# Kernel optimization log

Measured on AMD Instinct MI355X. Metric: run time of the kernel, lower is better.

Reference implementation:

```python
import jax, jax.numpy as jnp
import numpy as np


def setup_inputs() -> dict:
    key = jax.random.key(0)
    ks = jax.random.split(key, 7)
    B, S, D, R = 4, 4096, 1024, 16
    scale = 1.0 / np.sqrt(D)
    return {
        "x": jax.random.normal(ks[0], (B, S, D), dtype=jnp.float32),
        "W_qkv": jax.random.normal(ks[1], (3 * D, D), dtype=jnp.float32) * scale,
        "b_qkv": jax.random.normal(ks[2], (3 * D,), dtype=jnp.float32) * 0.02,
        "W_a_q": jax.random.normal(ks[3], (R, D), dtype=jnp.float32) * scale,
        "W_b_q": jnp.zeros((D, R), dtype=jnp.float32) + jax.random.normal(ks[4], (D, R), dtype=jnp.float32) * 0.02,
        "W_a_v": jax.random.normal(ks[5], (R, D), dtype=jnp.float32) * scale,
        "W_b_v": jax.random.normal(ks[6], (D, R), dtype=jnp.float32) * 0.02,
    }


def reference(x, W_qkv, b_qkv, W_a_q, W_b_q, W_a_v, W_b_v):
    D = W_a_q.shape[1]
    # base qkv projection: [B, S, 3D]
    qkv = jnp.einsum("bsd,ed->bse", x, W_qkv) + b_qkv
    # LoRA branches: x -> [B,S,r] -> [B,S,D]
    q_ba = jnp.einsum("bsr,dr->bsd", jnp.einsum("bsd,rd->bsr", x, W_a_q), W_b_q)
    v_ba = jnp.einsum("bsr,dr->bsd", jnp.einsum("bsd,rd->bsr", x, W_a_v), W_b_v)
    # add into q slice ([:D]) and v slice ([-D:])
    qkv = qkv.at[:, :, :D].add(q_ba)
    qkv = qkv.at[:, :, -D:].add(v_ba)
    return qkv
```

## Files before the change

### kernel.cpp

```cpp
#include <hip/hip_runtime.h>
#include <hip/hip_bf16.h>

typedef __bf16 bf16x4 __attribute__((ext_vector_type(4)));
typedef __bf16 bf16x8 __attribute__((ext_vector_type(8)));
typedef float floatx4 __attribute__((ext_vector_type(4)));

#define GLD16(gp, lp) __builtin_amdgcn_global_load_lds(                      \
    (const __attribute__((address_space(1))) void*)(gp),                     \
    (__attribute__((address_space(3))) void*)(lp), 16, 0, 0)

constexpr int Mdim = 16384;
constexpr int Ndim = 3072;
constexpr int Kdim = 1024;

static __device__ __forceinline__ bf16x8 cvt8(floatx4 lo, floatx4 hi) {
    bf16x8 r;
#pragma unroll
    for (int e = 0; e < 4; ++e) { r[e] = (__bf16)lo[e]; r[e + 4] = (__bf16)hi[e]; }
    return r;
}


__global__ __launch_bounds__(256) void build_weff(
    const float* __restrict__ Wqkv,
    const float* __restrict__ Waq,
    const float* __restrict__ Wbq,
    const float* __restrict__ Wav,
    const float* __restrict__ Wbv,
    __hip_bfloat16* __restrict__ Weff)
{
    const int idx = (blockIdx.x * 256 + threadIdx.x) * 4;
    const int e = idx >> 10;
    const int d = idx & 1023;
    floatx4 v = *(const floatx4*)(Wqkv + idx);
    if (e < 1024) {
#pragma unroll
        for (int r = 0; r < 16; ++r) {
            const float wb = Wbq[e * 16 + r];
            floatx4 wa = *(const floatx4*)(Waq + r * 1024 + d);
#pragma unroll
            for (int q = 0; q < 4; ++q) v[q] += wb * wa[q];
        }
    } else if (e >= 2048) {
        const int e2 = e - 2048;
#pragma unroll
        for (int r = 0; r < 16; ++r) {
            const float wb = Wbv[e2 * 16 + r];
            floatx4 wa = *(const floatx4*)(Wav + r * 1024 + d);
#pragma unroll
            for (int q = 0; q < 4; ++q) v[q] += wb * wa[q];
        }
    }
    bf16x4 o;
#pragma unroll
    for (int q = 0; q < 4; ++q) o[q] = (__bf16)v[q];
    *(bf16x4*)(Weff + idx) = o;
}

__global__ __launch_bounds__(256) void cvt_x(
    const float* __restrict__ x, __hip_bfloat16* __restrict__ xb)
{
    const size_t idx = ((size_t)blockIdx.x * 256 + threadIdx.x) * 8;
    bf16x8 r = cvt8(*(const floatx4*)(x + idx), *(const floatx4*)(x + idx + 4));
    *(bf16x8*)(xb + idx) = r;
}

__global__ __launch_bounds__(256, 3) void gemm_bf16(
    const __hip_bfloat16* __restrict__ A,
    const __hip_bfloat16* __restrict__ Bw,
    const float* __restrict__ bias,
    float* __restrict__ C)
{
    constexpr int TK = 32;
    __shared__ __hip_bfloat16 As[128 * TK];
    __shared__ __hip_bfloat16 Bs[128 * TK];

    const int t    = threadIdx.x;
    const int wave = t >> 6;
    const int lane = t & 63;
    const int bx   = blockIdx.x % (Ndim / 128);
    const int by   = blockIdx.x / (Ndim / 128);
    const int m0   = by * 128;
    const int n0   = bx * 128;
    const int wm   = wave >> 1;
    const int wn   = wave & 1;

    const int srow = wave * 16 + (lane >> 2);
    const int scol = (lane & 3) * 8;

    const __hip_bfloat16* Ag0 = A  + (size_t)(m0 + srow) * Kdim + scol;
    const __hip_bfloat16* Ag1 = Ag0 + (size_t)64 * Kdim;
    const __hip_bfloat16* Bg0 = Bw + (size_t)(n0 + srow) * Kdim + scol;
    const __hip_bfloat16* Bg1 = Bg0 + (size_t)64 * Kdim;

    __hip_bfloat16* Al0 = &As[srow * TK + scol];
    __hip_bfloat16* Al1 = &As[(srow + 64) * TK + scol];
    __hip_bfloat16* Bl0 = &Bs[srow * TK + scol];
    __hip_bfloat16* Bl1 = &Bs[(srow + 64) * TK + scol];

    const int fm = lane & 15;
    const int fk = (lane >> 4) * 8;

    floatx4 acc[4][4];
#pragma unroll
    for (int i = 0; i < 4; ++i)
#pragma unroll
        for (int j = 0; j < 4; ++j)
            acc[i][j] = (floatx4){0.f, 0.f, 0.f, 0.f};

    for (int kt = 0; kt < Kdim; kt += TK) {
        GLD16(Ag0 + kt, Al0);
        GLD16(Ag1 + kt, Al1);
        GLD16(Bg0 + kt, Bl0);
        GLD16(Bg1 + kt, Bl1);
        __syncthreads();

        bf16x8 af[4], bfr[4];
#pragma unroll
        for (int i = 0; i < 4; ++i) {
            af[i]  = *(const bf16x8*)&As[(wm * 64 + i * 16 + fm) * TK + fk];
            bfr[i] = *(const bf16x8*)&Bs[(wn * 64 + i * 16 + fm) * TK + fk];
        }
#pragma unroll
        for (int i = 0; i < 4; ++i)
#pragma unroll
            for (int j = 0; j < 4; ++j)
                acc[i][j] = __builtin_amdgcn_mfma_f32_16x16x32_bf16(af[i], bfr[j], acc[i][j], 0, 0, 0);
        __syncthreads();
    }

    const int cn = lane & 15;
    const int cm = (lane >> 4) * 4;
    float bv[4];
#pragma unroll
    for (int j = 0; j < 4; ++j)
        bv[j] = bias[n0 + wn * 64 + j * 16 + cn];

#pragma unroll
    for (int i = 0; i < 4; ++i) {
        const int m = m0 + wm * 64 + i * 16 + cm;
#pragma unroll
        for (int j = 0; j < 4; ++j) {
            const int n = n0 + wn * 64 + j * 16 + cn;
            const size_t base = (size_t)m * Ndim + n;
#pragma unroll
            for (int r = 0; r < 4; ++r)
                C[base + (size_t)r * Ndim] = acc[i][j][r] + bv[j];
        }
    }
}


__global__ __launch_bounds__(256, 2) void gemm_bias_f32(
    const float* __restrict__ A, const float* __restrict__ Bw,
    const float* __restrict__ bias, float* __restrict__ C)
{
    constexpr int TK = 32;
    __shared__ __hip_bfloat16 As[128 * TK];
    __shared__ __hip_bfloat16 Bs[128 * TK];

    const int t    = threadIdx.x;
    const int wave = t >> 6;
    const int lane = t & 63;
    const int bx   = blockIdx.x % (Ndim / 128);
    const int by   = blockIdx.x / (Ndim / 128);
    const int m0   = by * 128;
    const int n0   = bx * 128;
    const int wm   = wave >> 1;
    const int wn   = wave & 1;
    const int srow = wave * 16 + (lane >> 2);
    const int scol = (lane & 3) * 8;

    const float* Ag0 = A  + (size_t)(m0 + srow) * Kdim + scol;
    const float* Ag1 = Ag0 + (size_t)64 * Kdim;
    const float* Bg0 = Bw + (size_t)(n0 + srow) * Kdim + scol;
    const float* Bg1 = Bg0 + (size_t)64 * Kdim;

    __hip_bfloat16* Al0 = &As[srow * TK + scol];
    __hip_bfloat16* Al1 = &As[(srow + 64) * TK + scol];
    __hip_bfloat16* Bl0 = &Bs[srow * TK + scol];
    __hip_bfloat16* Bl1 = &Bs[(srow + 64) * TK + scol];

    const int fm = lane & 15;
    const int fk = (lane >> 4) * 8;

    floatx4 acc[4][4];
#pragma unroll
    for (int i = 0; i < 4; ++i)
#pragma unroll
        for (int j = 0; j < 4; ++j)
            acc[i][j] = (floatx4){0.f, 0.f, 0.f, 0.f};

    for (int kt = 0; kt < Kdim; kt += TK) {
        bf16x8 a0 = cvt8(*(const floatx4*)(Ag0 + kt), *(const floatx4*)(Ag0 + kt + 4));
        bf16x8 a1 = cvt8(*(const floatx4*)(Ag1 + kt), *(const floatx4*)(Ag1 + kt + 4));
        bf16x8 b0 = cvt8(*(const floatx4*)(Bg0 + kt), *(const floatx4*)(Bg0 + kt + 4));
        bf16x8 b1 = cvt8(*(const floatx4*)(Bg1 + kt), *(const floatx4*)(Bg1 + kt + 4));
        __syncthreads();
        *(bf16x8*)Al0 = a0;
        *(bf16x8*)Al1 = a1;
        *(bf16x8*)Bl0 = b0;
        *(bf16x8*)Bl1 = b1;
        __syncthreads();

        bf16x8 af[4], bfr[4];
#pragma unroll
        for (int i = 0; i < 4; ++i) {
            af[i]  = *(const bf16x8*)&As[(wm * 64 + i * 16 + fm) * TK + fk];
            bfr[i] = *(const bf16x8*)&Bs[(wn * 64 + i * 16 + fm) * TK + fk];
        }
#pragma unroll
        for (int i = 0; i < 4; ++i)
#pragma unroll
            for (int j = 0; j < 4; ++j)
                acc[i][j] = __builtin_amdgcn_mfma_f32_16x16x32_bf16(af[i], bfr[j], acc[i][j], 0, 0, 0);
    }

    const int cn = lane & 15;
    const int cm = (lane >> 4) * 4;
    float bv[4];
#pragma unroll
    for (int j = 0; j < 4; ++j)
        bv[j] = bias[n0 + wn * 64 + j * 16 + cn];
#pragma unroll
    for (int i = 0; i < 4; ++i) {
        const int m = m0 + wm * 64 + i * 16 + cm;
#pragma unroll
        for (int j = 0; j < 4; ++j) {
            const int n = n0 + wn * 64 + j * 16 + cn;
            const size_t base = (size_t)m * Ndim + n;
#pragma unroll
            for (int r = 0; r < 4; ++r)
                C[base + (size_t)r * Ndim] = acc[i][j][r] + bv[j];
        }
    }
}

__global__ __launch_bounds__(256) void lora_rmw(
    const float* __restrict__ x,
    const float* __restrict__ Waq, const float* __restrict__ Wbq,
    const float* __restrict__ Wav, const float* __restrict__ Wbv,
    float* __restrict__ out)
{
    __shared__ float Pq[64][16];
    __shared__ float Pv[64][16];
    const int t  = threadIdx.x;
    const int m0 = blockIdx.x * 64;
    {
        const int row = t >> 2;
        const int r0  = (t & 3) * 4;
        float accq[4] = {0.f, 0.f, 0.f, 0.f};
        float accv[4] = {0.f, 0.f, 0.f, 0.f};
        const float* xr = x + (size_t)(m0 + row) * Kdim;
        for (int d = 0; d < Kdim; d += 4) {
            floatx4 xv = *(const floatx4*)(xr + d);
#pragma unroll
            for (int rr = 0; rr < 4; ++rr) {
                floatx4 wq = *(const floatx4*)(Waq + (size_t)(r0 + rr) * Kdim + d);
                floatx4 wv = *(const floatx4*)(Wav + (size_t)(r0 + rr) * Kdim + d);
#pragma unroll
                for (int e = 0; e < 4; ++e) {
                    accq[rr] += xv[e] * wq[e];
                    accv[rr] += xv[e] * wv[e];
                }
            }
        }
#pragma unroll
        for (int rr = 0; rr < 4; ++rr) {
            Pq[row][r0 + rr] = accq[rr];
            Pv[row][r0 + rr] = accv[rr];
        }
    }
    __syncthreads();
    const int col  = t * 8;
    const bool isq = col < 1024;
    const int nn0  = isq ? col : col - 1024;
    const int n    = isq ? col : col + 1024;
    const float* Wb = isq ? Wbq : Wbv;
    for (int row = 0; row < 64; ++row) {
        const float* P = isq ? Pq[row] : Pv[row];
        const size_t off = (size_t)(m0 + row) * Ndim + n;
        floatx4 o0 = *(const floatx4*)(out + off);
        floatx4 o1 = *(const floatx4*)(out + off + 4);
#pragma unroll
        for (int i = 0; i < 8; ++i) {
            floatx4 w0 = *(const floatx4*)(Wb + (size_t)(nn0 + i) * 16);
            floatx4 w1 = *(const floatx4*)(Wb + (size_t)(nn0 + i) * 16 + 4);
            floatx4 w2 = *(const floatx4*)(Wb + (size_t)(nn0 + i) * 16 + 8);
            floatx4 w3 = *(const floatx4*)(Wb + (size_t)(nn0 + i) * 16 + 12);
            float s = 0.f;
#pragma unroll
            for (int r = 0; r < 4; ++r)
                s += P[r] * w0[r] + P[r + 4] * w1[r] + P[r + 8] * w2[r] + P[r + 12] * w3[r];
            if (i < 4) o0[i] += s; else o1[i - 4] += s;
        }
        *(floatx4*)(out + off)     = o0;
        *(floatx4*)(out + off + 4) = o1;
    }
}

extern "C" void kernel_launch(void* const* d_in, const int* in_sizes, int n_in,
                              void* d_out, int out_size, void* d_ws, size_t ws_size,
                              hipStream_t stream)
{
    (void)in_sizes; (void)n_in; (void)out_size;
    const float* x    = (const float*)d_in[0];
    const float* Wqkv = (const float*)d_in[1];
    const float* bqkv = (const float*)d_in[2];
    const float* Waq  = (const float*)d_in[3];
    const float* Wbq  = (const float*)d_in[4];
    const float* Wav  = (const float*)d_in[5];
    const float* Wbv  = (const float*)d_in[6];
    float* out = (float*)d_out;

    const size_t WEFF_BYTES = (size_t)Ndim * Kdim * sizeof(__hip_bfloat16);
    const size_t XB_BYTES   = (size_t)Mdim * Kdim * sizeof(__hip_bfloat16);

    if (ws_size >= WEFF_BYTES + XB_BYTES) {
        __hip_bfloat16* Weff = (__hip_bfloat16*)d_ws;
        __hip_bfloat16* xb   = (__hip_bfloat16*)((char*)d_ws + WEFF_BYTES);
        build_weff<<<(Ndim * Kdim / 4) / 256, 256, 0, stream>>>(Wqkv, Waq, Wbq, Wav, Wbv, Weff);
        cvt_x<<<(int)(((size_t)Mdim * Kdim / 8) / 256), 256, 0, stream>>>(x, xb);
        gemm_bf16<<<(Mdim / 128) * (Ndim / 128), 256, 0, stream>>>(xb, Weff, bqkv, out);
    } else {
        gemm_bias_f32<<<(Mdim / 128) * (Ndim / 128), 256, 0, stream>>>(x, Wqkv, bqkv, out);
        lora_rmw<<<Mdim / 64, 256, 0, stream>>>(x, Waq, Wbq, Wav, Wbv, out);
    }
}
```

Measured before the change: 382.2 us.

## Rewrite bf16 GEMM as 256x256 double-buffered 8-phase pipelined kernel

Replaces the 128x128, 256-thread, K-step-32 GEMM with a 256x256 tile kernel using 512 threads and K-step 64. Each K tile is double-buffered in LDS with an XOR swizzle. Global-to-LDS staging of the next tile is interleaved between four MFMA sub-phases, with s_setprio raising the priority of the MFMA sections. Block IDs are also remapped to improve L2 locality. The goal is to hide load latency, raise data reuse per LDS byte, and cut bank conflicts, at the cost of 128KB of LDS per block, which limits occupancy to one block per CU.

Measured after the change: 366.9 us. -4.0%, faster.

```diff
diff --git a/kernel.cpp b/kernel.cpp
--- a/kernel.cpp
+++ b/kernel.cpp
@@ -65,68 +65,116 @@
     *(bf16x8*)(xb + idx) = r;
 }
 
-__global__ __launch_bounds__(256, 3) void gemm_bf16(
+__global__ __launch_bounds__(512, 2) void gemm_bf16_8ph(
     const __hip_bfloat16* __restrict__ A,
     const __hip_bfloat16* __restrict__ Bw,
     const float* __restrict__ bias,
     float* __restrict__ C)
 {
-    constexpr int TK = 32;
-    __shared__ __hip_bfloat16 As[128 * TK];
-    __shared__ __hip_bfloat16 Bs[128 * TK];
+    constexpr int NT = Kdim / 64;
+    __shared__ __hip_bfloat16 lds[2][2][256 * 64];
 
     const int t    = threadIdx.x;
-    const int wave = t >> 6;
+    const int wid  = t >> 6;
     const int lane = t & 63;
-    const int bx   = blockIdx.x % (Ndim / 128);
-    const int by   = blockIdx.x / (Ndim / 128);
-    const int m0   = by * 128;
-    const int n0   = bx * 128;
-    const int wm   = wave >> 1;
-    const int wn   = wave & 1;
-
-    const int srow = wave * 16 + (lane >> 2);
-    const int scol = (lane & 3) * 8;
-
-    const __hip_bfloat16* Ag0 = A  + (size_t)(m0 + srow) * Kdim + scol;
-    const __hip_bfloat16* Ag1 = Ag0 + (size_t)64 * Kdim;
-    const __hip_bfloat16* Bg0 = Bw + (size_t)(n0 + srow) * Kdim + scol;
-    const __hip_bfloat16* Bg1 = Bg0 + (size_t)64 * Kdim;
-
-    __hip_bfloat16* Al0 = &As[srow * TK + scol];
-    __hip_bfloat16* Al1 = &As[(srow + 64) * TK + scol];
-    __hip_bfloat16* Bl0 = &Bs[srow * TK + scol];
-    __hip_bfloat16* Bl1 = &Bs[(srow + 64) * TK + scol];
-
-    const int fm = lane & 15;
-    const int fk = (lane >> 4) * 8;
-
-    floatx4 acc[4][4];
-#pragma unroll
-    for (int i = 0; i < 4; ++i)
+    const int wm   = wid >> 2;
+    const int wn   = wid & 3;
+
+    constexpr int NWG = (Mdim / 256) * (Ndim / 256);
+    const int bid = (blockIdx.x & 7) * (NWG >> 3) + (blockIdx.x >> 3);
+    const int bx  = bid % (Ndim / 256);
+    const int by  = bid / (Ndim / 256);
+    const int m0  = by * 256;
+    const int n0  = bx * 256;
+
+    const int srow0 = t >> 3;
+    const int scb_s = ((t & 7) * 16) ^ ((srow0 & 7) << 4);
+
+#define STAGE_HALF(G, R0, h, nb_, mat, kt_) do {                               \
+    const __hip_bfloat16* _g = (G) + (size_t)((R0) + (h) * 128 + srow0) * Kdim \
+                               + (kt_) * 64 + (scb_s >> 1);                    \
+    char* _l = (char*)&lds[nb_][mat][0] + (h) * 16384 + t * 16;                \
+    GLD16(_g, _l);                                                             \
+    GLD16(_g + (size_t)64 * Kdim, _l + 8192);                                  \
+} while (0)
+
+    const int fm   = lane & 15;
+    const int fk2  = (lane >> 4) * 16;
+    const int fxor = (fm & 7) << 4;
+    const int cbs0 = fk2 ^ fxor;
+    const int cbs1 = (64 + fk2) ^ fxor;
+
+    floatx4 acc[8][4];
+#pragma unroll
+    for (int i = 0; i < 8; ++i)
 #pragma unroll
         for (int j = 0; j < 4; ++j)
             acc[i][j] = (floatx4){0.f, 0.f, 0.f, 0.f};
 
-    for (int kt = 0; kt < Kdim; kt += TK) {
-        GLD16(Ag0 + kt, Al0);
-        GLD16(Ag1 + kt, Al1);
-        GLD16(Bg0 + kt, Bl0);
-        GLD16(Bg1 + kt, Bl1);
-        __syncthreads();
-
-        bf16x8 af[4], bfr[4];
-#pragma unroll
-        for (int i = 0; i < 4; ++i) {
-            af[i]  = *(const bf16x8*)&As[(wm * 64 + i * 16 + fm) * TK + fk];
-            bfr[i] = *(const bf16x8*)&Bs[(wn * 64 + i * 16 + fm) * TK + fk];
-        }
-#pragma unroll
-        for (int i = 0; i < 4; ++i)
-#pragma unroll
-            for (int j = 0; j < 4; ++j)
-                acc[i][j] = __builtin_amdgcn_mfma_f32_16x16x32_bf16(af[i], bfr[j], acc[i][j], 0, 0, 0);
-        __syncthreads();
+#define MFMA_QUAD(mq, nq, BQ)                                                  \
+    __builtin_amdgcn_s_setprio(1);                                             \
+    _Pragma("unroll")                                                          \
+    for (int i = 0; i < 4; ++i)                                                \
+        _Pragma("unroll")                                                      \
+        for (int j = 0; j < 2; ++j) {                                          \
+            acc[(mq) * 4 + i][(nq) * 2 + j] =                                  \
+                __builtin_amdgcn_mfma_f32_16x16x32_bf16(                       \
+                    aq[i][0], BQ[j][0], acc[(mq) * 4 + i][(nq) * 2 + j], 0, 0, 0); \
+            acc[(mq) * 4 + i][(nq) * 2 + j] =                                  \
+                __builtin_amdgcn_mfma_f32_16x16x32_bf16(                       \
+                    aq[i][1], BQ[j][1], acc[(mq) * 4 + i][(nq) * 2 + j], 0, 0, 0); \
+        }                                                                      \
+    __builtin_amdgcn_s_setprio(0);
+
+    STAGE_HALF(A,  m0, 0, 0, 0, 0);
+    STAGE_HALF(A,  m0, 1, 0, 0, 0);
+    STAGE_HALF(Bw, n0, 0, 0, 1, 0);
+    STAGE_HALF(Bw, n0, 1, 0, 1, 0);
+
+    bf16x8 aq[4][2], bq0[2][2], bq1[2][2];
+
+    for (int kt = 0; kt < NT; ++kt) {
+        const int nb = kt & 1;
+        const char* Ab = (const char*)&lds[nb][0][0];
+        const char* Bb = (const char*)&lds[nb][1][0];
+
+#define LDA8(i, mq, kk) (*(const bf16x8*)(Ab + ((wm * 128 + (mq) * 64 + (i) * 16 + fm) * 128 + cbs##kk)))
+#define LDB8(j, nq, kk) (*(const bf16x8*)(Bb + ((wn * 64 + (nq) * 32 + (j) * 16 + fm) * 128 + cbs##kk)))
+
+        if (kt + 1 < NT) {
+            STAGE_HALF(A,  m0, 0, nb ^ 1, 0, kt + 1);
+            STAGE_HALF(Bw, n0, 0, nb ^ 1, 1, kt + 1);
+            asm volatile("s_waitcnt vmcnt(4)" ::: "memory");
+        } else {
+            asm volatile("s_waitcnt vmcnt(0)" ::: "memory");
+        }
+        __builtin_amdgcn_s_barrier();
+#pragma unroll
+        for (int i = 0; i < 4; ++i) { aq[i][0] = LDA8(i, 0, 0); aq[i][1] = LDA8(i, 0, 1); }
+#pragma unroll
+        for (int j = 0; j < 2; ++j) { bq0[j][0] = LDB8(j, 0, 0); bq0[j][1] = LDB8(j, 0, 1); }
+        MFMA_QUAD(0, 0, bq0)
+        __builtin_amdgcn_s_barrier();
+
+#pragma unroll
+        for (int j = 0; j < 2; ++j) { bq1[j][0] = LDB8(j, 1, 0); bq1[j][1] = LDB8(j, 1, 1); }
+        if (kt + 1 < NT) STAGE_HALF(A, m0, 1, nb ^ 1, 0, kt + 1);
+        __builtin_amdgcn_s_barrier();
+        MFMA_QUAD(0, 1, bq1)
+        __builtin_amdgcn_s_barrier();
+
+#pragma unroll
+        for (int i = 0; i < 4; ++i) { aq[i][0] = LDA8(i, 1, 0); aq[i][1] = LDA8(i, 1, 1); }
+        if (kt + 1 < NT) STAGE_HALF(Bw, n0, 1, nb ^ 1, 1, kt + 1);
+        __builtin_amdgcn_s_barrier();
+        MFMA_QUAD(1, 0, bq0)
+        __builtin_amdgcn_s_barrier();
+
+        MFMA_QUAD(1, 1, bq1)
+        __builtin_amdgcn_s_barrier();
+
+#undef LDA8
+#undef LDB8
     }
 
     const int cn = lane & 15;
@@ -137,17 +185,19 @@
         bv[j] = bias[n0 + wn * 64 + j * 16 + cn];
 
 #pragma unroll
-    for (int i = 0; i < 4; ++i) {
-        const int m = m0 + wm * 64 + i * 16 + cm;
-#pragma unroll
-        for (int j = 0; j < 4; ++j) {
-            const int n = n0 + wn * 64 + j * 16 + cn;
+    for (int mi = 0; mi < 8; ++mi) {
+        const int m = m0 + wm * 128 + mi * 16 + cm;
+#pragma unroll
+        for (int ni = 0; ni < 4; ++ni) {
+            const int n = n0 + wn * 64 + ni * 16 + cn;
             const size_t base = (size_t)m * Ndim + n;
 #pragma unroll
             for (int r = 0; r < 4; ++r)
-                C[base + (size_t)r * Ndim] = acc[i][j][r] + bv[j];
-        }
-    }
+                C[base + (size_t)r * Ndim] = acc[mi][ni][r] + bv[ni];
+        }
+    }
+#undef STAGE_HALF
+#undef MFMA_QUAD
 }
 
 
@@ -321,7 +371,7 @@
         __hip_bfloat16* xb   = (__hip_bfloat16*)((char*)d_ws + WEFF_BYTES);
         build_weff<<<(Ndim * Kdim / 4) / 256, 256, 0, stream>>>(Wqkv, Waq, Wbq, Wav, Wbv, Weff);
         cvt_x<<<(int)(((size_t)Mdim * Kdim / 8) / 256), 256, 0, stream>>>(x, xb);
-        gemm_bf16<<<(Mdim / 128) * (Ndim / 128), 256, 0, stream>>>(xb, Weff, bqkv, out);
+        gemm_bf16_8ph<<<(Mdim / 256) * (Ndim / 256), 512, 0, stream>>>(xb, Weff, bqkv, out);
     } else {
         gemm_bias_f32<<<(Mdim / 128) * (Ndim / 128), 256, 0, stream>>>(x, Wqkv, bqkv, out);
         lora_rmw<<<Mdim / 64, 256, 0, stream>>>(x, Waq, Wbq, Wav, Wbv, out);
```

## Double-buffer bf16 GEMM with 64-wide K tiles, XOR-swizzled LDS and block remap

Applied to the files above, without the earlier changes.

Rewrites the main bf16 GEMM to use a K tile of 64 with two LDS buffers. The next tile's global-to-LDS loads are issued while MFMAs run on the current one. LDS columns are XOR-swizzled to avoid bank conflicts, and block IDs are remapped in groups of 8 to change L2 locality. It also raises MFMA priority with s_setprio. The cost is 64KB of LDS and occupancy reduced to 2 blocks per CU.

New measurement: 372.9 us. 1.02x faster.

```diff
diff --git a/kernel.cpp b/kernel.cpp
--- a/kernel.cpp
+++ b/kernel.cpp
@@ -65,41 +65,53 @@
     *(bf16x8*)(xb + idx) = r;
 }
 
-__global__ __launch_bounds__(256, 3) void gemm_bf16(
+__global__ __launch_bounds__(256, 2) void gemm_bf16_v3(
     const __hip_bfloat16* __restrict__ A,
     const __hip_bfloat16* __restrict__ Bw,
     const float* __restrict__ bias,
     float* __restrict__ C)
 {
-    constexpr int TK = 32;
-    __shared__ __hip_bfloat16 As[128 * TK];
-    __shared__ __hip_bfloat16 Bs[128 * TK];
+    constexpr int NT = Kdim / 64;
+    __shared__ __hip_bfloat16 lds[2][2][128 * 64];
 
     const int t    = threadIdx.x;
     const int wave = t >> 6;
     const int lane = t & 63;
-    const int bx   = blockIdx.x % (Ndim / 128);
-    const int by   = blockIdx.x / (Ndim / 128);
-    const int m0   = by * 128;
-    const int n0   = bx * 128;
     const int wm   = wave >> 1;
     const int wn   = wave & 1;
 
-    const int srow = wave * 16 + (lane >> 2);
-    const int scol = (lane & 3) * 8;
-
-    const __hip_bfloat16* Ag0 = A  + (size_t)(m0 + srow) * Kdim + scol;
-    const __hip_bfloat16* Ag1 = Ag0 + (size_t)64 * Kdim;
-    const __hip_bfloat16* Bg0 = Bw + (size_t)(n0 + srow) * Kdim + scol;
-    const __hip_bfloat16* Bg1 = Bg0 + (size_t)64 * Kdim;
-
-    __hip_bfloat16* Al0 = &As[srow * TK + scol];
-    __hip_bfloat16* Al1 = &As[(srow + 64) * TK + scol];
-    __hip_bfloat16* Bl0 = &Bs[srow * TK + scol];
-    __hip_bfloat16* Bl1 = &Bs[(srow + 64) * TK + scol];
-
-    const int fm = lane & 15;
-    const int fk = (lane >> 4) * 8;
+    constexpr int NWG = (Mdim / 128) * (Ndim / 128);
+    const int bid = (blockIdx.x & 7) * (NWG >> 3) + (blockIdx.x >> 3);
+    const int bx  = bid % (Ndim / 128);
+    const int by  = bid / (Ndim / 128);
+    const int m0  = by * 128;
+    const int n0  = bx * 128;
+
+    const int srow0 = t >> 3;
+    const int scb_s = ((t & 7) * 16) ^ ((srow0 & 7) << 4);
+
+#define STAGE_TILE(nb_, kt_) do {                                              \
+    const __hip_bfloat16* _ga = A  + (size_t)(m0 + srow0) * Kdim               \
+                                + (kt_) * 64 + (scb_s >> 1);                   \
+    const __hip_bfloat16* _gb = Bw + (size_t)(n0 + srow0) * Kdim               \
+                                + (kt_) * 64 + (scb_s >> 1);                   \
+    char* _la = (char*)&lds[nb_][0][0] + t * 16;                               \
+    char* _lb = (char*)&lds[nb_][1][0] + t * 16;                               \
+    GLD16(_ga,                      _la);                                      \
+    GLD16(_ga + (size_t)32 * Kdim,  _la + 4096);                               \
+    GLD16(_ga + (size_t)64 * Kdim,  _la + 8192);                               \
+    GLD16(_ga + (size_t)96 * Kdim,  _la + 12288);                              \
+    GLD16(_gb,                      _lb);                                      \
+    GLD16(_gb + (size_t)32 * Kdim,  _lb + 4096);                               \
+    GLD16(_gb + (size_t)64 * Kdim,  _lb + 8192);                               \
+    GLD16(_gb + (size_t)96 * Kdim,  _lb + 12288);                              \
+} while (0)
+
+    const int fm   = lane & 15;
+    const int fk2  = (lane >> 4) * 16;
+    const int fxor = (fm & 7) << 4;
+    const int cbs0 = fk2 ^ fxor;
+    const int cbs1 = (64 + fk2) ^ fxor;
 
     floatx4 acc[4][4];
 #pragma unroll
@@ -108,25 +120,40 @@
         for (int j = 0; j < 4; ++j)
             acc[i][j] = (floatx4){0.f, 0.f, 0.f, 0.f};
 
-    for (int kt = 0; kt < Kdim; kt += TK) {
-        GLD16(Ag0 + kt, Al0);
-        GLD16(Ag1 + kt, Al1);
-        GLD16(Bg0 + kt, Bl0);
-        GLD16(Bg1 + kt, Bl1);
-        __syncthreads();
-
-        bf16x8 af[4], bfr[4];
+    STAGE_TILE(0, 0);
+
+    for (int kt = 0; kt < NT; ++kt) {
+        const int nb = kt & 1;
+        if (kt + 1 < NT) {
+            STAGE_TILE(nb ^ 1, kt + 1);
+            asm volatile("s_waitcnt vmcnt(8)" ::: "memory");
+        } else {
+            asm volatile("s_waitcnt vmcnt(0)" ::: "memory");
+        }
+        __builtin_amdgcn_s_barrier();
+
+        const char* Ab = (const char*)&lds[nb][0][0];
+        const char* Bb = (const char*)&lds[nb][1][0];
+        bf16x8 aq[2][4], bq[2][4];
 #pragma unroll
         for (int i = 0; i < 4; ++i) {
-            af[i]  = *(const bf16x8*)&As[(wm * 64 + i * 16 + fm) * TK + fk];
-            bfr[i] = *(const bf16x8*)&Bs[(wn * 64 + i * 16 + fm) * TK + fk];
-        }
-#pragma unroll
-        for (int i = 0; i < 4; ++i)
-#pragma unroll
-            for (int j = 0; j < 4; ++j)
-                acc[i][j] = __builtin_amdgcn_mfma_f32_16x16x32_bf16(af[i], bfr[j], acc[i][j], 0, 0, 0);
-        __syncthreads();
+            aq[0][i] = *(const bf16x8*)(Ab + (wm * 64 + i * 16 + fm) * 128 + cbs0);
+            aq[1][i] = *(const bf16x8*)(Ab + (wm * 64 + i * 16 + fm) * 128 + cbs1);
+            bq[0][i] = *(const bf16x8*)(Bb + (wn * 64 + i * 16 + fm) * 128 + cbs0);
+            bq[1][i] = *(const bf16x8*)(Bb + (wn * 64 + i * 16 + fm) * 128 + cbs1);
+        }
+        __builtin_amdgcn_s_setprio(1);
+#pragma unroll
+        for (int kk = 0; kk < 2; ++kk)
+#pragma unroll
+            for (int i = 0; i < 4; ++i)
+#pragma unroll
+                for (int j = 0; j < 4; ++j)
+                    acc[i][j] = __builtin_amdgcn_mfma_f32_16x16x32_bf16(
+                        aq[kk][i], bq[kk][j], acc[i][j], 0, 0, 0);
+        __builtin_amdgcn_s_setprio(0);
+        if (kt + 1 < NT)
+            __builtin_amdgcn_s_barrier();
     }
 
     const int cn = lane & 15;
@@ -148,6 +175,7 @@
                 C[base + (size_t)r * Ndim] = acc[i][j][r] + bv[j];
         }
     }
+#undef STAGE_TILE
 }
 
 
@@ -321,7 +349,7 @@
         __hip_bfloat16* xb   = (__hip_bfloat16*)((char*)d_ws + WEFF_BYTES);
         build_weff<<<(Ndim * Kdim / 4) / 256, 256, 0, stream>>>(Wqkv, Waq, Wbq, Wav, Wbv, Weff);
         cvt_x<<<(int)(((size_t)Mdim * Kdim / 8) / 256), 256, 0, stream>>>(x, xb);
-        gemm_bf16<<<(Mdim / 128) * (Ndim / 128), 256, 0, stream>>>(xb, Weff, bqkv, out);
+        gemm_bf16_v3<<<(Mdim / 128) * (Ndim / 128), 256, 0, stream>>>(xb, Weff, bqkv, out);
     } else {
         gemm_bias_f32<<<(Mdim / 128) * (Ndim / 128), 256, 0, stream>>>(x, Wqkv, bqkv, out);
         lora_rmw<<<Mdim / 64, 256, 0, stream>>>(x, Waq, Wbq, Wav, Wbv, out);
```
